# Optimization experiments

Measured on AMD Instinct MI355X. Metric: run time of the kernel, lower is better.

The kernel has to match this reference:

```python
import jax, jax.numpy as jnp
import numpy as np

D_MODEL = 1024
NHEAD = 16
HEAD_DIM = D_MODEL // NHEAD


def setup_inputs() -> dict:
    key = jax.random.key(0)
    ks = jax.random.split(key, 11)
    B, S = 4, 2048
    s = 1.0 / np.sqrt(D_MODEL)
    return {
        "q": jax.random.normal(ks[0], (B, S, D_MODEL), jnp.float32),
        "k": jax.random.normal(ks[1], (B, S, D_MODEL), jnp.float32),
        "v": jax.random.normal(ks[2], (B, S, D_MODEL), jnp.float32),
        "Wq": jax.random.normal(ks[3], (D_MODEL, D_MODEL), jnp.float32) * s,
        "bq": jnp.zeros((D_MODEL,), jnp.float32),
        "Wk": jax.random.normal(ks[4], (D_MODEL, D_MODEL), jnp.float32) * s,
        "bk": jnp.zeros((D_MODEL,), jnp.float32),
        "Wv": jax.random.normal(ks[5], (D_MODEL, D_MODEL), jnp.float32) * s,
        "bv": jnp.zeros((D_MODEL,), jnp.float32),
        "Wo": jax.random.normal(ks[6], (D_MODEL, D_MODEL), jnp.float32) * s,
        "bo": jnp.zeros((D_MODEL,), jnp.float32),
    }


def reference(q, k, v, Wq, bq, Wk, bk, Wv, bv, Wo, bo):
    B, S, _ = q.shape
    H, Dh = NHEAD, HEAD_DIM

    def proj(x, W, b):  # nn.Linear: x @ W.T + b, then split heads -> [B,H,S,Dh]
        y = x @ W.T + b
        return y.reshape(B, S, H, Dh).transpose(0, 2, 1, 3)

    qh = proj(q, Wq, bq)
    kh = proj(k, Wk, bk)
    vh = proj(v, Wv, bv)

    scores = jnp.einsum("bhsd,bhtd->bhst", qh, kh) / jnp.sqrt(jnp.float32(Dh))
    attn = jax.nn.softmax(scores, axis=-1)
    out = jnp.einsum("bhst,bhtd->bhsd", attn, vh)  # [B,H,S,Dh]
    out = out.transpose(0, 2, 1, 3).reshape(B, S, H * Dh)
    return out @ Wo.T + bo
```

## Files before the change

kernel.cpp:

```cpp
#include <hip/hip_runtime.h>


typedef short bf16x8 __attribute__((ext_vector_type(8)));
typedef short bf16x4 __attribute__((ext_vector_type(4)));
typedef float f32x4 __attribute__((ext_vector_type(4)));

__device__ __forceinline__ short f2bf(float x) {
    union { float f; unsigned int u; } un; un.f = x;
    unsigned int u = un.u;
    return (short)(unsigned short)((u + 0x7fffu + ((u >> 16) & 1u)) >> 16);
}

__device__ __forceinline__ void gll16(const void* g, void* l) {
    __builtin_amdgcn_global_load_lds(
        (const __attribute__((address_space(1))) void*)g,
        (__attribute__((address_space(3))) void*)l, 16, 0, 0);
}

struct CvtArgs { const float* s[4]; unsigned short* d[4]; int n4; };
__global__ __launch_bounds__(256) void cvt_bf16(CvtArgs ca) {
    const float* s = ca.s[blockIdx.y];
    unsigned short* d = ca.d[blockIdx.y];
    int i = blockIdx.x * blockDim.x + threadIdx.x;
    int stride = gridDim.x * blockDim.x;
    const float4* s4 = reinterpret_cast<const float4*>(s);
    bf16x4* d4 = reinterpret_cast<bf16x4*>(d);
    for (; i < ca.n4; i += stride) {
        float4 x = s4[i];
        bf16x4 y;
        y[0] = f2bf(x.x); y[1] = f2bf(x.y); y[2] = f2bf(x.z); y[3] = f2bf(x.w);
        d4[i] = y;
    }
}

__device__ __forceinline__ void gemm_core(const unsigned short* __restrict__ A,
                                          const unsigned short* __restrict__ W,
                                          const float* __restrict__ bias,
                                          float scale, void* __restrict__ out,
                                          int mode) {
    __shared__ unsigned short As[128 * 64];
    __shared__ unsigned short Bs[128 * 64];
    const int tid = threadIdx.x;
    const int m0 = blockIdx.y * 128, n0 = blockIdx.x * 128;
    const int wave = tid >> 6, lane = tid & 63;
    const int wm = (wave >> 1) * 64, wn = (wave & 1) * 64;
    const int l15 = lane & 15, quad = lane >> 4;
    const int srow = tid >> 3;
    const int scol = ((tid & 7) ^ (srow & 7)) * 8;
    const int cb = (l15 & 7);

    f32x4 acc[4][4] = {};

    for (int k0 = 0; k0 < 1024; k0 += 64) {
        __syncthreads();
#pragma unroll
        for (int ro = 0; ro < 4; ++ro) {
            gll16(&A[(size_t)(m0 + ro * 32 + srow) * 1024 + k0 + scol], &As[ro * 2048 + tid * 8]);
            gll16(&W[(size_t)(n0 + ro * 32 + srow) * 1024 + k0 + scol], &Bs[ro * 2048 + tid * 8]);
        }
        __syncthreads();
#pragma unroll
        for (int kk = 0; kk < 2; ++kk) {
            const int co = ((4 * kk + quad) ^ cb) * 8;
            bf16x8 a[4], b[4];
#pragma unroll
            for (int i = 0; i < 4; ++i)
                a[i] = *reinterpret_cast<bf16x8*>(&As[(wm + i * 16 + l15) * 64 + co]);
#pragma unroll
            for (int j = 0; j < 4; ++j)
                b[j] = *reinterpret_cast<bf16x8*>(&Bs[(wn + j * 16 + l15) * 64 + co]);
#pragma unroll
            for (int i = 0; i < 4; ++i)
#pragma unroll
                for (int j = 0; j < 4; ++j)
                    acc[i][j] = __builtin_amdgcn_mfma_f32_16x16x32_bf16(a[i], b[j], acc[i][j], 0, 0, 0);
        }
    }

#pragma unroll
    for (int i = 0; i < 4; ++i) {
#pragma unroll
        for (int j = 0; j < 4; ++j) {
#pragma unroll
            for (int r = 0; r < 4; ++r) {
                int m = m0 + wm + i * 16 + quad * 4 + r;
                int n = n0 + wn + j * 16 + l15;
                float val = (acc[i][j][r] + bias[n]) * scale;
                if (mode == 0) {
                    reinterpret_cast<float*>(out)[(size_t)m * 1024 + n] = val;
                } else {
                    int b_ = m >> 11, s = m & 2047, h = n >> 6, d = n & 63;
                    size_t off = (mode == 1)
                                     ? ((size_t)((b_ * 16 + h) * 2048 + s) * 64 + d)
                                     : ((size_t)((b_ * 16 + h) * 64 + d) * 2048 + s);
                    reinterpret_cast<unsigned short*>(out)[off] = (unsigned short)f2bf(val);
                }
            }
        }
    }
}

struct QkvArgs {
    const unsigned short* A[3];
    const unsigned short* W[3];
    const float* bias[3];
    float scale[3];
    unsigned short* out[3];
    int mode[3];
};
__global__ __launch_bounds__(256) void gemm_qkv(QkvArgs ga) {
    int z = blockIdx.z;
    gemm_core(ga.A[z], ga.W[z], ga.bias[z], ga.scale[z], ga.out[z], ga.mode[z]);
}

__global__ __launch_bounds__(256) void gemm_wo(const unsigned short* __restrict__ A,
                                               const unsigned short* __restrict__ W,
                                               const float* __restrict__ bias,
                                               float* __restrict__ out) {
    gemm_core(A, W, bias, 1.0f, out, 0);
}

__global__ __launch_bounds__(256, 3) void flash_attn(const unsigned short* __restrict__ Qh,
                                                     const unsigned short* __restrict__ Kh,
                                                     const unsigned short* __restrict__ Vt,
                                                     unsigned short* __restrict__ Oa) {
    constexpr int LD = 72;
    __shared__ unsigned short Ks[2][64 * 64];
    __shared__ unsigned short Vs[2][64 * 64];
    __shared__ unsigned short Ps[4 * 32 * LD];
    const int tid = threadIdx.x;
    const int bh = blockIdx.y;
    const int q0 = blockIdx.x * 128;
    const unsigned short* Qb = Qh + (size_t)bh * 2048 * 64;
    const unsigned short* Kb = Kh + (size_t)bh * 2048 * 64;
    const unsigned short* Vb = Vt + (size_t)bh * 64 * 2048;
    const int wave = tid >> 6, lane = tid & 63;
    const int l15 = lane & 15, quad = lane >> 4;
    const int wq = wave * 32;
    const int srow = tid >> 3;
    const int scol = ((tid & 7) ^ (srow & 7)) * 8;
    const int cb = (l15 & 7);
    unsigned short* Pw = &Ps[wave * 32 * LD];

    bf16x8 qreg[2][2];
#pragma unroll
    for (int i = 0; i < 2; ++i)
#pragma unroll
        for (int kk = 0; kk < 2; ++kk)
            qreg[i][kk] = *reinterpret_cast<const bf16x8*>(
                &Qb[(size_t)(q0 + wq + i * 16 + l15) * 64 + kk * 32 + quad * 8]);

    bf16x8 ones;
#pragma unroll
    for (int j = 0; j < 8; ++j) ones[j] = (short)0x3F80;

    f32x4 o[2][4] = {};
    f32x4 lacc[2] = {};

#pragma unroll
    for (int ro = 0; ro < 2; ++ro) {
        gll16(&Kb[(size_t)(ro * 32 + srow) * 64 + scol], &Ks[0][ro * 2048 + tid * 8]);
        gll16(&Vb[(size_t)(ro * 32 + srow) * 2048 + scol], &Vs[0][ro * 2048 + tid * 8]);
    }
    __syncthreads();

    for (int it = 0; it < 32; ++it) {
        const int buf = it & 1;
        if (it < 31) {
            int kvn = (it + 1) * 64;
#pragma unroll
            for (int ro = 0; ro < 2; ++ro) {
                gll16(&Kb[(size_t)(kvn + ro * 32 + srow) * 64 + scol], &Ks[buf ^ 1][ro * 2048 + tid * 8]);
                gll16(&Vb[(size_t)(ro * 32 + srow) * 2048 + kvn + scol], &Vs[buf ^ 1][ro * 2048 + tid * 8]);
            }
        }

        f32x4 sacc[2][4] = {};
#pragma unroll
        for (int kk = 0; kk < 2; ++kk) {
            const int co = ((4 * kk + quad) ^ cb) * 8;
            bf16x8 ak[4];
#pragma unroll
            for (int j = 0; j < 4; ++j)
                ak[j] = *reinterpret_cast<bf16x8*>(&Ks[buf][(j * 16 + l15) * 64 + co]);
#pragma unroll
            for (int i = 0; i < 2; ++i)
#pragma unroll
                for (int j = 0; j < 4; ++j)
                    sacc[i][j] = __builtin_amdgcn_mfma_f32_16x16x32_bf16(ak[j], qreg[i][kk], sacc[i][j], 0, 0, 0);
        }

#pragma unroll
        for (int i = 0; i < 2; ++i) {
#pragma unroll
            for (int j = 0; j < 4; ++j) {
                float p0 = __builtin_amdgcn_exp2f(sacc[i][j][0]);
                float p1 = __builtin_amdgcn_exp2f(sacc[i][j][1]);
                float p2 = __builtin_amdgcn_exp2f(sacc[i][j][2]);
                float p3 = __builtin_amdgcn_exp2f(sacc[i][j][3]);
                union { float f; unsigned u; } a0{p0}, a1{p1}, a2{p2}, a3{p3};
                unsigned lo = __builtin_amdgcn_perm(a1.u + 0x8000u, a0.u + 0x8000u, 0x07060302u);
                unsigned hi = __builtin_amdgcn_perm(a3.u + 0x8000u, a2.u + 0x8000u, 0x07060302u);
                uint2 pk; pk.x = lo; pk.y = hi;
                *reinterpret_cast<uint2*>(&Pw[(i * 16 + l15) * LD + j * 16 + quad * 4]) = pk;
            }
        }

#pragma unroll
        for (int kk = 0; kk < 2; ++kk) {
            const int co = ((4 * kk + quad) ^ cb) * 8;
            bf16x8 ap[2];
#pragma unroll
            for (int i = 0; i < 2; ++i)
                ap[i] = *reinterpret_cast<bf16x8*>(&Pw[(i * 16 + l15) * LD + kk * 32 + quad * 8]);
#pragma unroll
            for (int i = 0; i < 2; ++i)
                lacc[i] = __builtin_amdgcn_mfma_f32_16x16x32_bf16(ap[i], ones, lacc[i], 0, 0, 0);
#pragma unroll
            for (int n = 0; n < 4; ++n) {
                bf16x8 bv = *reinterpret_cast<bf16x8*>(&Vs[buf][(n * 16 + l15) * 64 + co]);
#pragma unroll
                for (int i = 0; i < 2; ++i)
                    o[i][n] = __builtin_amdgcn_mfma_f32_16x16x32_bf16(ap[i], bv, o[i][n], 0, 0, 0);
            }
        }
        __syncthreads();
    }

    const int b_ = bh >> 4, h = bh & 15;
#pragma unroll
    for (int i = 0; i < 2; ++i) {
        f32x4 rv;
#pragma unroll
        for (int r = 0; r < 4; ++r) rv[r] = 1.0f / lacc[i][r];
#pragma unroll
        for (int n = 0; n < 4; ++n)
#pragma unroll
            for (int r = 0; r < 4; ++r) {
                int s = q0 + wq + i * 16 + quad * 4 + r;
                int d = n * 16 + l15;
                Oa[(size_t)(b_ * 2048 + s) * 1024 + h * 64 + d] =
                    (unsigned short)f2bf(o[i][n][r] * rv[r]);
            }
    }
}

extern "C" void kernel_launch(void* const* d_in, const int* in_sizes, int n_in,
                              void* d_out, int out_size, void* d_ws, size_t ws_size,
                              hipStream_t stream) {
    const float* q  = (const float*)d_in[0];
    const float* k  = (const float*)d_in[1];
    const float* v  = (const float*)d_in[2];
    const float* Wq = (const float*)d_in[3];
    const float* bq = (const float*)d_in[4];
    const float* Wk = (const float*)d_in[5];
    const float* bk = (const float*)d_in[6];
    const float* Wv = (const float*)d_in[7];
    const float* bv = (const float*)d_in[8];
    const float* Wo = (const float*)d_in[9];
    const float* bo = (const float*)d_in[10];

    const size_t E = (size_t)8192 * 1024;
    const size_t WE = (size_t)1024 * 1024;
    unsigned short* r0 = (unsigned short*)d_ws;
    unsigned short* r1 = r0 + E;
    unsigned short* r2 = r1 + E;
    unsigned short* r3 = r2 + E;
    unsigned short* wqb = r3 + E;
    unsigned short* wkb = wqb + WE;
    unsigned short* wvb = wkb + WE;
    unsigned short* wob = wvb + WE;

    CvtArgs ca;
    ca.s[0] = q; ca.d[0] = r0;
    ca.s[1] = k; ca.d[1] = r1;
    ca.s[2] = v; ca.d[2] = r2;
    ca.s[3] = q; ca.d[3] = r0;
    ca.n4 = (int)(E / 4);
    cvt_bf16<<<dim3(1024, 3), 256, 0, stream>>>(ca);

    CvtArgs cw;
    cw.s[0] = Wq; cw.d[0] = wqb;
    cw.s[1] = Wk; cw.d[1] = wkb;
    cw.s[2] = Wv; cw.d[2] = wvb;
    cw.s[3] = Wo; cw.d[3] = wob;
    cw.n4 = (int)(WE / 4);
    cvt_bf16<<<dim3(256, 4), 256, 0, stream>>>(cw);

    const float QSCALE = 0.125f * 1.44269504088896340736f;

    QkvArgs ga;
    ga.A[0] = r0; ga.W[0] = wqb; ga.bias[0] = bq; ga.scale[0] = QSCALE; ga.out[0] = r3; ga.mode[0] = 1;
    ga.A[1] = r1; ga.W[1] = wkb; ga.bias[1] = bk; ga.scale[1] = 1.0f;   ga.out[1] = r0; ga.mode[1] = 1;
    ga.A[2] = r2; ga.W[2] = wvb; ga.bias[2] = bv; ga.scale[2] = 1.0f;   ga.out[2] = r1; ga.mode[2] = 2;
    gemm_qkv<<<dim3(8, 64, 3), 256, 0, stream>>>(ga);

    flash_attn<<<dim3(16, 64), 256, 0, stream>>>(r3, r0, r1, r2);
    gemm_wo<<<dim3(8, 64), 256, 0, stream>>>(r2, wob, bo, (float*)d_out);
}
```

Measured before the change: 374.1 us.

## Enlarge GEMM tiles with double-buffered K-loop and retile flash attention to 8 waves

The GEMM core becomes templated with larger 256x256 and 256x128 tiles, a 32-wide K step, and double-buffered shared memory so the next tile loads while MFMAs run. The B operand is now staged through registers instead of direct-to-LDS loads. Flash attention moves to 512-thread blocks covering 256 queries, with 32-key KV tiles and K and V loads split across the two thread halves. The aim is more reuse per load and overlap of loads with compute, at the cost of higher register pressure, fewer blocks in the grid, and a barrier every smaller K step.

Measured after the change: 397.2 us. 1.06x slower.

```diff
diff --git a/kernel.cpp b/kernel.cpp
--- a/kernel.cpp
+++ b/kernel.cpp
@@ -33,54 +33,80 @@
     }
 }
 
+template <int TM, int TN>
 __device__ __forceinline__ void gemm_core(const unsigned short* __restrict__ A,
                                           const unsigned short* __restrict__ W,
                                           const float* __restrict__ bias,
                                           float scale, void* __restrict__ out,
                                           int mode) {
-    __shared__ unsigned short As[128 * 64];
-    __shared__ unsigned short Bs[128 * 64];
+    constexpr int NWM = TM / 64, NWN = TN / 128;
+    constexpr int NT = NWM * NWN * 64;
+    constexpr int CA = TM * 4;
+    constexpr int CB = TN * 4;
+    __shared__ unsigned short As[2][TM * 32];
+    __shared__ unsigned short Bs[2][TN * 32];
     const int tid = threadIdx.x;
-    const int m0 = blockIdx.y * 128, n0 = blockIdx.x * 128;
+    const int m0 = blockIdx.y * TM, n0 = blockIdx.x * TN;
     const int wave = tid >> 6, lane = tid & 63;
-    const int wm = (wave >> 1) * 64, wn = (wave & 1) * 64;
+    const int wm = (wave % NWM) * 64, wn = (wave / NWM) * 128;
     const int l15 = lane & 15, quad = lane >> 4;
-    const int srow = tid >> 3;
-    const int scol = ((tid & 7) ^ (srow & 7)) * 8;
-    const int cb = (l15 & 7);
-
-    f32x4 acc[4][4] = {};
-
-    for (int k0 = 0; k0 < 1024; k0 += 64) {
+
+    f32x4 acc[4][8] = {};
+
+#define STAGE_A(K0, PB)                                                           \
+    {                                                                             \
+        _Pragma("unroll") for (int c0 = 0; c0 < CA; c0 += NT) {                   \
+            int c = c0 + tid;                                                     \
+            int row = c >> 2, ch = (c & 3) ^ (row & 3);                           \
+            gll16(&A[(size_t)(m0 + row) * 1024 + (K0) + ch * 8], &As[PB][c * 8]); \
+        }                                                                         \
+    }
+#define STAGE_B(K0, PB)                                                           \
+    {                                                                             \
+        _Pragma("unroll") for (int c0 = 0; c0 < CB; c0 += NT) {                   \
+            int c = c0 + tid;                                                     \
+            int row = c >> 2, ch = (c & 3) ^ (row & 3);                           \
+            *reinterpret_cast<bf16x8*>(&Bs[PB][c * 8]) =                          \
+                *reinterpret_cast<const bf16x8*>(                                 \
+                    &W[(size_t)(n0 + row) * 1024 + (K0) + ch * 8]);               \
+        }                                                                         \
+    }
+
+    STAGE_A(0, 0);
+    STAGE_B(0, 0);
+    __syncthreads();
+
+    for (int it = 0; it < 32; ++it) {
+        const int pb = it & 1;
+        if (it < 31) {
+            STAGE_A((it + 1) * 32, pb ^ 1);
+            STAGE_B((it + 1) * 32, pb ^ 1);
+        }
+        bf16x8 a[4], b[8];
+#pragma unroll
+        for (int i = 0; i < 4; ++i) {
+            int row = wm + i * 16 + l15;
+            a[i] = *reinterpret_cast<bf16x8*>(&As[pb][row * 32 + (quad ^ (row & 3)) * 8]);
+        }
+#pragma unroll
+        for (int j = 0; j < 8; ++j) {
+            int row = wn + j * 16 + l15;
+            b[j] = *reinterpret_cast<bf16x8*>(&Bs[pb][row * 32 + (quad ^ (row & 3)) * 8]);
+        }
+#pragma unroll
+        for (int i = 0; i < 4; ++i)
+#pragma unroll
+            for (int j = 0; j < 8; ++j)
+                acc[i][j] = __builtin_amdgcn_mfma_f32_16x16x32_bf16(a[i], b[j], acc[i][j], 0, 0, 0);
         __syncthreads();
-#pragma unroll
-        for (int ro = 0; ro < 4; ++ro) {
-            gll16(&A[(size_t)(m0 + ro * 32 + srow) * 1024 + k0 + scol], &As[ro * 2048 + tid * 8]);
-            gll16(&W[(size_t)(n0 + ro * 32 + srow) * 1024 + k0 + scol], &Bs[ro * 2048 + tid * 8]);
-        }
-        __syncthreads();
-#pragma unroll
-        for (int kk = 0; kk < 2; ++kk) {
-            const int co = ((4 * kk + quad) ^ cb) * 8;
-            bf16x8 a[4], b[4];
-#pragma unroll
-            for (int i = 0; i < 4; ++i)
-                a[i] = *reinterpret_cast<bf16x8*>(&As[(wm + i * 16 + l15) * 64 + co]);
-#pragma unroll
-            for (int j = 0; j < 4; ++j)
-                b[j] = *reinterpret_cast<bf16x8*>(&Bs[(wn + j * 16 + l15) * 64 + co]);
-#pragma unroll
-            for (int i = 0; i < 4; ++i)
-#pragma unroll
-                for (int j = 0; j < 4; ++j)
-                    acc[i][j] = __builtin_amdgcn_mfma_f32_16x16x32_bf16(a[i], b[j], acc[i][j], 0, 0, 0);
-        }
-    }
+    }
+#undef STAGE_A
+#undef STAGE_B
 
 #pragma unroll
     for (int i = 0; i < 4; ++i) {
 #pragma unroll
-        for (int j = 0; j < 4; ++j) {
+        for (int j = 0; j < 8; ++j) {
 #pragma unroll
             for (int r = 0; r < 4; ++r) {
                 int m = m0 + wm + i * 16 + quad * 4 + r;
@@ -108,39 +134,49 @@
     unsigned short* out[3];
     int mode[3];
 };
-__global__ __launch_bounds__(256) void gemm_qkv(QkvArgs ga) {
+__global__ __launch_bounds__(512, 2) void gemm_qkv(QkvArgs ga) {
     int z = blockIdx.z;
-    gemm_core(ga.A[z], ga.W[z], ga.bias[z], ga.scale[z], ga.out[z], ga.mode[z]);
-}
-
-__global__ __launch_bounds__(256) void gemm_wo(const unsigned short* __restrict__ A,
-                                               const unsigned short* __restrict__ W,
-                                               const float* __restrict__ bias,
-                                               float* __restrict__ out) {
-    gemm_core(A, W, bias, 1.0f, out, 0);
-}
-
-__global__ __launch_bounds__(256, 3) void flash_attn(const unsigned short* __restrict__ Qh,
+    gemm_core<256, 256>(ga.A[z], ga.W[z], ga.bias[z], ga.scale[z], ga.out[z], ga.mode[z]);
+}
+
+__global__ __launch_bounds__(256, 2) void gemm_wo(const unsigned short* __restrict__ A,
+                                                  const unsigned short* __restrict__ W,
+                                                  const float* __restrict__ bias,
+                                                  float* __restrict__ out) {
+    gemm_core<256, 128>(A, W, bias, 1.0f, out, 0);
+}
+
+__global__ __launch_bounds__(512, 4) void flash_attn(const unsigned short* __restrict__ Qh,
                                                      const unsigned short* __restrict__ Kh,
                                                      const unsigned short* __restrict__ Vt,
                                                      unsigned short* __restrict__ Oa) {
-    constexpr int LD = 72;
-    __shared__ unsigned short Ks[2][64 * 64];
-    __shared__ unsigned short Vs[2][64 * 64];
-    __shared__ unsigned short Ps[4 * 32 * LD];
+    constexpr int LD = 40;
+    __shared__ unsigned short Ks[2][32 * 64];
+    __shared__ unsigned short Vs[2][64 * 32];
+    __shared__ unsigned short Ps[8][32 * LD];
     const int tid = threadIdx.x;
     const int bh = blockIdx.y;
-    const int q0 = blockIdx.x * 128;
+    const int q0 = blockIdx.x * 256;
     const unsigned short* Qb = Qh + (size_t)bh * 2048 * 64;
     const unsigned short* Kb = Kh + (size_t)bh * 2048 * 64;
     const unsigned short* Vb = Vt + (size_t)bh * 64 * 2048;
     const int wave = tid >> 6, lane = tid & 63;
     const int l15 = lane & 15, quad = lane >> 4;
     const int wq = wave * 32;
-    const int srow = tid >> 3;
-    const int scol = ((tid & 7) ^ (srow & 7)) * 8;
-    const int cb = (l15 & 7);
-    unsigned short* Pw = &Ps[wave * 32 * LD];
+    unsigned short* Pw = Ps[wave];
+
+    const int stK = tid < 256;
+    const int su = tid & 255;
+    const int krow = su >> 3, kch = (su & 7) ^ (krow & 7);
+    const int vrow = su >> 2, vch = (su & 3) ^ (vrow & 3);
+
+#define STAGE_KV(KV0, PB)                                                        \
+    {                                                                            \
+        if (stK)                                                                 \
+            gll16(&Kb[(size_t)((KV0) + krow) * 64 + kch * 8], &Ks[PB][su * 8]);  \
+        else                                                                     \
+            gll16(&Vb[(size_t)vrow * 2048 + (KV0) + vch * 8], &Vs[PB][su * 8]);  \
+    }
 
     bf16x8 qreg[2][2];
 #pragma unroll
@@ -157,43 +193,34 @@
     f32x4 o[2][4] = {};
     f32x4 lacc[2] = {};
 
-#pragma unroll
-    for (int ro = 0; ro < 2; ++ro) {
-        gll16(&Kb[(size_t)(ro * 32 + srow) * 64 + scol], &Ks[0][ro * 2048 + tid * 8]);
-        gll16(&Vb[(size_t)(ro * 32 + srow) * 2048 + scol], &Vs[0][ro * 2048 + tid * 8]);
-    }
+    STAGE_KV(0, 0);
     __syncthreads();
 
-    for (int it = 0; it < 32; ++it) {
-        const int buf = it & 1;
-        if (it < 31) {
-            int kvn = (it + 1) * 64;
-#pragma unroll
-            for (int ro = 0; ro < 2; ++ro) {
-                gll16(&Kb[(size_t)(kvn + ro * 32 + srow) * 64 + scol], &Ks[buf ^ 1][ro * 2048 + tid * 8]);
-                gll16(&Vb[(size_t)(ro * 32 + srow) * 2048 + kvn + scol], &Vs[buf ^ 1][ro * 2048 + tid * 8]);
+    for (int it = 0; it < 64; ++it) {
+        const int pb = it & 1;
+        if (it < 63) STAGE_KV((it + 1) * 32, pb ^ 1);
+
+        f32x4 sacc[2][2] = {};
+#pragma unroll
+        for (int kk = 0; kk < 2; ++kk) {
+            bf16x8 ak[2];
+#pragma unroll
+            for (int j = 0; j < 2; ++j) {
+                int row = j * 16 + l15;
+                ak[j] = *reinterpret_cast<bf16x8*>(
+                    &Ks[pb][row * 64 + (((kk * 4 + quad) ^ (row & 7)) * 8)]);
             }
-        }
-
-        f32x4 sacc[2][4] = {};
-#pragma unroll
-        for (int kk = 0; kk < 2; ++kk) {
-            const int co = ((4 * kk + quad) ^ cb) * 8;
-            bf16x8 ak[4];
-#pragma unroll
-            for (int j = 0; j < 4; ++j)
-                ak[j] = *reinterpret_cast<bf16x8*>(&Ks[buf][(j * 16 + l15) * 64 + co]);
 #pragma unroll
             for (int i = 0; i < 2; ++i)
 #pragma unroll
-                for (int j = 0; j < 4; ++j)
+                for (int j = 0; j < 2; ++j)
                     sacc[i][j] = __builtin_amdgcn_mfma_f32_16x16x32_bf16(ak[j], qreg[i][kk], sacc[i][j], 0, 0, 0);
         }
 
 #pragma unroll
         for (int i = 0; i < 2; ++i) {
 #pragma unroll
-            for (int j = 0; j < 4; ++j) {
+            for (int j = 0; j < 2; ++j) {
                 float p0 = __builtin_amdgcn_exp2f(sacc[i][j][0]);
                 float p1 = __builtin_amdgcn_exp2f(sacc[i][j][1]);
                 float p2 = __builtin_amdgcn_exp2f(sacc[i][j][2]);
@@ -206,26 +233,25 @@
             }
         }
 
-#pragma unroll
-        for (int kk = 0; kk < 2; ++kk) {
-            const int co = ((4 * kk + quad) ^ cb) * 8;
-            bf16x8 ap[2];
+        bf16x8 ap[2];
+#pragma unroll
+        for (int i = 0; i < 2; ++i)
+            ap[i] = *reinterpret_cast<bf16x8*>(&Pw[(i * 16 + l15) * LD + quad * 8]);
+#pragma unroll
+        for (int i = 0; i < 2; ++i)
+            lacc[i] = __builtin_amdgcn_mfma_f32_16x16x32_bf16(ap[i], ones, lacc[i], 0, 0, 0);
+#pragma unroll
+        for (int n = 0; n < 4; ++n) {
+            int row = n * 16 + l15;
+            bf16x8 bv = *reinterpret_cast<bf16x8*>(
+                &Vs[pb][row * 32 + ((quad ^ (row & 3)) * 8)]);
 #pragma unroll
             for (int i = 0; i < 2; ++i)
-                ap[i] = *reinterpret_cast<bf16x8*>(&Pw[(i * 16 + l15) * LD + kk * 32 + quad * 8]);
-#pragma unroll
-            for (int i = 0; i < 2; ++i)
-                lacc[i] = __builtin_amdgcn_mfma_f32_16x16x32_bf16(ap[i], ones, lacc[i], 0, 0, 0);
-#pragma unroll
-            for (int n = 0; n < 4; ++n) {
-                bf16x8 bv = *reinterpret_cast<bf16x8*>(&Vs[buf][(n * 16 + l15) * 64 + co]);
-#pragma unroll
-                for (int i = 0; i < 2; ++i)
-                    o[i][n] = __builtin_amdgcn_mfma_f32_16x16x32_bf16(ap[i], bv, o[i][n], 0, 0, 0);
-            }
+                o[i][n] = __builtin_amdgcn_mfma_f32_16x16x32_bf16(ap[i], bv, o[i][n], 0, 0, 0);
         }
         __syncthreads();
     }
+#undef STAGE_KV
 
     const int b_ = bh >> 4, h = bh & 15;
 #pragma unroll
@@ -293,8 +319,8 @@
     ga.A[0] = r0; ga.W[0] = wqb; ga.bias[0] = bq; ga.scale[0] = QSCALE; ga.out[0] = r3; ga.mode[0] = 1;
     ga.A[1] = r1; ga.W[1] = wkb; ga.bias[1] = bk; ga.scale[1] = 1.0f;   ga.out[1] = r0; ga.mode[1] = 1;
     ga.A[2] = r2; ga.W[2] = wvb; ga.bias[2] = bv; ga.scale[2] = 1.0f;   ga.out[2] = r1; ga.mode[2] = 2;
-    gemm_qkv<<<dim3(8, 64, 3), 256, 0, stream>>>(ga);
-
-    flash_attn<<<dim3(16, 64), 256, 0, stream>>>(r3, r0, r1, r2);
-    gemm_wo<<<dim3(8, 64), 256, 0, stream>>>(r2, wob, bo, (float*)d_out);
-}
+    gemm_qkv<<<dim3(4, 32, 3), 512, 0, stream>>>(ga);
+
+    flash_attn<<<dim3(8, 64), 512, 0, stream>>>(r3, r0, r1, r2);
+    gemm_wo<<<dim3(8, 32), 256, 0, stream>>>(r2, wob, bo, (float*)d_out);
+}
```
